# Kernel tuning notes

Hardware: AMD Instinct MI355X
Metric: run time of the kernel (lower is better)

The kernel has to match this reference:

```python
import jax, jax.numpy as jnp
import numpy as np

B, D, E, H, L = 32768, 512, 10, 128, 2  # batch, input_dim, max_charts, expert hidden, latent_dim
RH1, RH2 = 256, 128                      # router hidden sizes
TAU = 3.0


def setup_inputs() -> dict:
    key = jax.random.key(0)
    ks = jax.random.split(key, 16)
    rnd = lambda k, *s: (jax.random.normal(k, s, jnp.float32) * 0.05)
    return {
        "x": jax.random.normal(ks[0], (B, D), jnp.float32),
        "u": jax.random.uniform(ks[1], (B, E), jnp.float32),
        # router params (last layer init ~ N(0, 0.01), bias 0, as in _init_router)
        "rw1": rnd(ks[2], D, RH1), "rb1": jnp.zeros((RH1,), jnp.float32),
        "rw2": rnd(ks[3], RH1, RH2), "rb2": jnp.zeros((RH2,), jnp.float32),
        "rw3": jax.random.normal(ks[4], (RH2, E), jnp.float32) * 0.01,
        "rb3": jnp.zeros((E,), jnp.float32),
        # stacked expert params: all 10 experts batched along leading dim
        "ew1": rnd(ks[5], E, D, H), "eb1": rnd(ks[6], E, H),
        "ew2": rnd(ks[7], E, H, H), "eb2": rnd(ks[8], E, H),
        "ew3": rnd(ks[9], E, H, L), "eb3": rnd(ks[10], E, L),
    }


def reference(x, u, rw1, rb1, rw2, rb2, rw3, rb3, ew1, eb1, ew2, eb2, ew3, eb3):
    # router MLP: D -> 256 -> 128 -> E
    h = jax.nn.relu(x @ rw1 + rb1)
    h = jax.nn.relu(h @ rw2 + rb2)
    logits = h @ rw3 + rb3                                  # [B, E]
    # gumbel_softmax(tau=3.0, hard=False): softmax((logits + gumbel)/tau)
    g = -jnp.log(-jnp.log(jnp.clip(u, 1e-10, 1.0)) + 1e-10)
    weights = jax.nn.softmax((logits + g) / TAU, axis=1)    # [B, E]
    # all 10 experts as batched GEMMs (fuses the python loop over charts)
    h1 = jax.nn.relu(jnp.einsum('bi,eio->beo', x, ew1) + eb1[None])   # [B, E, H]
    h2 = jax.nn.relu(jnp.einsum('beh,eho->beo', h1, ew2) + eb2[None]) # [B, E, H]
    zc = jnp.einsum('beh,ehl->bel', h2, ew3) + eb3[None]              # [B, E, L]
    z = jnp.einsum('be,bel->bl', weights, zc)                         # [B, L]
    chart_outputs = jnp.transpose(zc, (1, 0, 2))                      # [E, B, L]
    return z, weights, chart_outputs
```

## Files before the change

kernel.cpp:

```cpp
#include <hip/hip_runtime.h>
#include <stdint.h>

typedef __bf16 bf16x8 __attribute__((ext_vector_type(8)));
typedef float floatx4 __attribute__((ext_vector_type(4)));
typedef unsigned short ushort_t;

__device__ __forceinline__ ushort_t bf16rne(float f) {
    union { float f; unsigned u; } v; v.f = f;
    return (ushort_t)((v.u + 0x7fffu + ((v.u >> 16) & 1u)) >> 16);
}

__device__ __forceinline__ void gl_lds16(const ushort_t* g, ushort_t* l) {
    __builtin_amdgcn_global_load_lds(
        (const __attribute__((address_space(1))) unsigned int*)g,
        (__attribute__((address_space(3))) unsigned int*)l, 16, 0, 0);
}


__global__ void prep(const float* __restrict__ x, ushort_t* __restrict__ x16,
                     const float* __restrict__ ew1, ushort_t* __restrict__ ew1t,
                     const float* __restrict__ ew2, ushort_t* __restrict__ ew2t,
                     const float* __restrict__ rw1, ushort_t* __restrict__ rw1t,
                     const float* __restrict__ rw2, ushort_t* __restrict__ rw2t) {
    __shared__ ushort_t sT[64 * 65];
    int b = blockIdx.x, tid = threadIdx.x;
    if (b < 16384) {
        int i = b * 256 + tid;
        float4 f = ((const float4*)x)[i];
        union { ushort_t s[4]; uint2 v; } pk;
        pk.s[0] = bf16rne(f.x); pk.s[1] = bf16rne(f.y);
        pk.s[2] = bf16rne(f.z); pk.s[3] = bf16rne(f.w);
        ((uint2*)x16)[i] = pk.v;
        return;
    }
    const float* in; ushort_t* outp; int K, N, k0, n0;
    int i = b - 16384;
    if (i < 160) {
        int e = i >> 4, t = i & 15;
        in = ew1 + e * 65536; outp = ew1t + e * 65536;
        K = 512; N = 128; k0 = (t >> 1) * 64; n0 = (t & 1) * 64;
    } else if (i < 200) {
        i -= 160; int e = i >> 2, t = i & 3;
        in = ew2 + e * 16384; outp = ew2t + e * 16384;
        K = 128; N = 128; k0 = (t >> 1) * 64; n0 = (t & 1) * 64;
    } else if (i < 232) {
        i -= 200; in = rw1; outp = rw1t;
        K = 512; N = 256; k0 = (i >> 2) * 64; n0 = (i & 3) * 64;
    } else {
        i -= 232; in = rw2; outp = rw2t;
        K = 256; N = 128; k0 = (i >> 1) * 64; n0 = (i & 1) * 64;
    }
    {
        int c = tid & 63, r0 = tid >> 6;
#pragma unroll
        for (int p = 0; p < 16; ++p) {
            int r = r0 * 16 + p;
            sT[c * 65 + r] = bf16rne(in[(size_t)(k0 + r) * N + n0 + c]);
        }
        __syncthreads();
        int rr = tid & 63, c0 = tid >> 6;
#pragma unroll
        for (int p = 0; p < 16; ++p) {
            int cc = c0 * 16 + p;
            outp[(size_t)(n0 + cc) * K + k0 + rr] = sT[cc * 65 + rr];
        }
    }
}

__global__ __launch_bounds__(256, 2)
void router_fused(const ushort_t* __restrict__ x16, const ushort_t* __restrict__ rw1t,
                  const float* __restrict__ rb1, const ushort_t* __restrict__ rw2t,
                  const float* __restrict__ rb2, const float* __restrict__ rw3,
                  const float* __restrict__ rb3, const float* __restrict__ u,
                  float* __restrict__ wts, float* __restrict__ z) {
    __shared__ alignas(16) ushort_t sStage[8192];
    __shared__ alignas(16) ushort_t sH1[16384];
    __shared__ float sw3[1280];
    __shared__ float sB1[128];
    __shared__ float sB2[128];
    __shared__ float lgbuf[128][10];

    const int tid = threadIdx.x;
    const int rb = blockIdx.x;
    const int wave = tid >> 6, lane = tid & 63;
    const int ln15 = lane & 15, q = lane >> 4;
    const int wm = (wave & 1) * 64, wn = (wave >> 1) * 64;
    const int mhalf = wm >> 6, nhalf = wn >> 6;

    for (int i = tid; i < 1280; i += 256) sw3[i] = rw3[i];
    if (tid < 128) sB2[tid] = rb2[tid];

    const ushort_t* xblk = x16 + (size_t)rb * 128 * 512;
    const int rl = lane >> 2, cl = lane & 3;
    const int sw = (cl ^ ((rl >> 1) & 3)) * 8;
    const int rg0 = wave * 2, rg1 = rg0 + 1;
    const int fslot = (4 * ln15 + (q ^ ((ln15 >> 1) & 3))) * 8;

    floatx4 acc2[4][4];
#pragma unroll
    for (int i = 0; i < 4; ++i)
#pragma unroll
        for (int j = 0; j < 4; ++j) acc2[i][j] = (floatx4){0.f, 0.f, 0.f, 0.f};

    for (int ph = 0; ph < 2; ++ph) {
        if (tid < 128) sB1[tid] = rb1[ph * 128 + tid];
        const ushort_t* w1base = rw1t + (size_t)ph * 128 * 512;

        floatx4 acc[4][4];
#pragma unroll
        for (int i = 0; i < 4; ++i)
#pragma unroll
            for (int j = 0; j < 4; ++j) acc[i][j] = (floatx4){0.f, 0.f, 0.f, 0.f};

        for (int k0 = 0; k0 < 512; k0 += 32) {
            __syncthreads();
            gl_lds16(xblk + (size_t)(rg0 * 16 + rl) * 512 + k0 + sw, &sStage[rg0 * 512]);
            gl_lds16(xblk + (size_t)(rg1 * 16 + rl) * 512 + k0 + sw, &sStage[rg1 * 512]);
            gl_lds16(w1base + (size_t)(rg0 * 16 + rl) * 512 + k0 + sw, &sStage[4096 + rg0 * 512]);
            gl_lds16(w1base + (size_t)(rg1 * 16 + rl) * 512 + k0 + sw, &sStage[4096 + rg1 * 512]);
            __syncthreads();
            bf16x8 a[4], b[4];
#pragma unroll
            for (int t = 0; t < 4; ++t) a[t] = *(const bf16x8*)(&sStage[4096 + (mhalf * 4 + t) * 512 + fslot]);
#pragma unroll
            for (int t = 0; t < 4; ++t) b[t] = *(const bf16x8*)(&sStage[(nhalf * 4 + t) * 512 + fslot]);
#pragma unroll
            for (int i = 0; i < 4; ++i)
#pragma unroll
                for (int j = 0; j < 4; ++j)
                    acc[i][j] = __builtin_amdgcn_mfma_f32_16x16x32_bf16(a[i], b[j], acc[i][j], 0, 0, 0);
        }

#pragma unroll
        for (int i = 0; i < 4; ++i) {
            int hbase = wm + 16 * i;
            int kh = hbase >> 5;
            int qhi = (hbase >> 4) & 1;
            int slotq = 2 * qhi + (q >> 1);
            int h0 = hbase + q * 4;
#pragma unroll
            for (int j = 0; j < 4; ++j) {
                union { ushort_t s[4]; uint2 v; } pk;
#pragma unroll
                for (int r = 0; r < 4; ++r)
                    pk.s[r] = bf16rne(fmaxf(acc[i][j][r] + sB1[h0 + r], 0.f));
                *(uint2*)(&sH1[kh * 4096 + (nhalf * 4 + j) * 512 + slotq * 128 + ln15 * 8 + (q & 1) * 4]) = pk.v;
            }
        }

        for (int p = 0; p < 2; ++p) {
            __syncthreads();
#pragma unroll
            for (int r = 0; r < 4; ++r) {
                int s = wave * 4 + r;
                int khl = s >> 3, rg = s & 7;
                int kh = p * 2 + khl;
                gl_lds16(rw2t + (size_t)(rg * 16 + rl) * 256 + ph * 128 + kh * 32 + sw, &sStage[s * 512]);
            }
            __syncthreads();
#pragma unroll
            for (int khl = 0; khl < 2; ++khl) {
                int kh = p * 2 + khl;
                bf16x8 a[4], b[4];
#pragma unroll
                for (int t = 0; t < 4; ++t) a[t] = *(const bf16x8*)(&sStage[(khl * 8 + mhalf * 4 + t) * 512 + fslot]);
#pragma unroll
                for (int t = 0; t < 4; ++t) b[t] = *(const bf16x8*)(&sH1[kh * 4096 + (nhalf * 4 + t) * 512 + lane * 8]);
#pragma unroll
                for (int i = 0; i < 4; ++i)
#pragma unroll
                    for (int j = 0; j < 4; ++j)
                        acc2[i][j] = __builtin_amdgcn_mfma_f32_16x16x32_bf16(a[i], b[j], acc2[i][j], 0, 0, 0);
            }
        }
    }

    float lg[4][10];
#pragma unroll
    for (int j = 0; j < 4; ++j)
#pragma unroll
        for (int ee = 0; ee < 10; ++ee) lg[j][ee] = 0.f;
#pragma unroll
    for (int i = 0; i < 4; ++i) {
#pragma unroll
        for (int r = 0; r < 4; ++r) {
            int n = wm + i * 16 + q * 4 + r;
            float bias = sB2[n];
            const float* w3r = &sw3[n * 10];
#pragma unroll
            for (int j = 0; j < 4; ++j) {
                float val = fmaxf(acc2[i][j][r] + bias, 0.f);
#pragma unroll
                for (int ee = 0; ee < 10; ++ee) lg[j][ee] += val * w3r[ee];
            }
        }
    }
#pragma unroll
    for (int j = 0; j < 4; ++j)
#pragma unroll
        for (int ee = 0; ee < 10; ++ee) {
            lg[j][ee] += __shfl_xor(lg[j][ee], 16, 64);
            lg[j][ee] += __shfl_xor(lg[j][ee], 32, 64);
        }
    if (wm == 0 && q == 0) {
#pragma unroll
        for (int j = 0; j < 4; ++j) {
            int row = wn + 16 * j + ln15;
#pragma unroll
            for (int ee = 0; ee < 10; ++ee) lgbuf[row][ee] = lg[j][ee];
        }
    }
    __syncthreads();
    if (wm == 64 && q == 0) {
#pragma unroll
        for (int j = 0; j < 4; ++j) {
            int row = wn + 16 * j + ln15;
#pragma unroll
            for (int ee = 0; ee < 10; ++ee) lgbuf[row][ee] += lg[j][ee];
        }
    }
    __syncthreads();
    if (tid < 128) {
        int grow = rb * 128 + tid;
        float v[10], mx = -1e30f;
#pragma unroll
        for (int ee = 0; ee < 10; ++ee) {
            float uu = u[(size_t)grow * 10 + ee];
            uu = fminf(fmaxf(uu, 1e-10f), 1.0f);
            float g = -logf(-logf(uu) + 1e-10f);
            v[ee] = (lgbuf[tid][ee] + rb3[ee] + g) * (1.0f / 3.0f);
            mx = fmaxf(mx, v[ee]);
        }
        float s = 0.f;
#pragma unroll
        for (int ee = 0; ee < 10; ++ee) { v[ee] = expf(v[ee] - mx); s += v[ee]; }
        float inv = 1.0f / s;
#pragma unroll
        for (int ee = 0; ee < 10; ++ee) wts[(size_t)grow * 10 + ee] = v[ee] * inv;
    }
    z[rb * 256 + tid] = 0.f;
}

__global__ __launch_bounds__(256, 3)
void expert_fused(const ushort_t* __restrict__ x16, const ushort_t* __restrict__ ew1t,
                  const ushort_t* __restrict__ ew2t, const float* __restrict__ eb1,
                  const float* __restrict__ eb2, const float* __restrict__ ew3,
                  const float* __restrict__ eb3, const float* __restrict__ wts,
                  float* __restrict__ chart, float* __restrict__ z) {
    __shared__ alignas(16) ushort_t sXW[8192];
    __shared__ alignas(16) ushort_t sH1[16384];
    __shared__ float sB1[128];
    __shared__ float sB2[128];
    __shared__ float sW3[256];
    __shared__ float zbuf[128][2];

    const int tid = threadIdx.x;
    const int id = blockIdx.x;
    const int xcd = id & 7, local = id >> 3;
    const int e = local % 10;
    const int rb = xcd * 32 + local / 10;

    const int wave = tid >> 6, lane = tid & 63;
    const int ln15 = lane & 15, q = lane >> 4;
    const int wm = (wave & 1) * 64, wn = (wave >> 1) * 64;
    const int mhalf = wm >> 6, nhalf = wn >> 6;

    if (tid < 128) sB1[tid] = eb1[e * 128 + tid];
    else sB2[tid - 128] = eb2[e * 128 + (tid - 128)];
    sW3[tid] = ew3[e * 256 + tid];

    const ushort_t* xblk = x16 + (size_t)rb * 128 * 512;
    const ushort_t* w1 = ew1t + (size_t)e * 128 * 512;
    const ushort_t* w2 = ew2t + (size_t)e * 128 * 128;

    const int rl = lane >> 2, cl = lane & 3;
    const int sw = (cl ^ ((rl >> 1) & 3)) * 8;
    const int rg0 = wave * 2, rg1 = rg0 + 1;
    const int fslot = (4 * ln15 + (q ^ ((ln15 >> 1) & 3))) * 8;

    {
        floatx4 acc[4][4];
#pragma unroll
        for (int i = 0; i < 4; ++i)
#pragma unroll
            for (int j = 0; j < 4; ++j) acc[i][j] = (floatx4){0.f, 0.f, 0.f, 0.f};

        for (int k0 = 0; k0 < 512; k0 += 32) {
            __syncthreads();
            gl_lds16(xblk + (size_t)(rg0 * 16 + rl) * 512 + k0 + sw, &sXW[rg0 * 512]);
            gl_lds16(xblk + (size_t)(rg1 * 16 + rl) * 512 + k0 + sw, &sXW[rg1 * 512]);
            gl_lds16(w1 + (size_t)(rg0 * 16 + rl) * 512 + k0 + sw, &sXW[4096 + rg0 * 512]);
            gl_lds16(w1 + (size_t)(rg1 * 16 + rl) * 512 + k0 + sw, &sXW[4096 + rg1 * 512]);
            __syncthreads();
            bf16x8 a[4], b[4];
#pragma unroll
            for (int t = 0; t < 4; ++t) a[t] = *(const bf16x8*)(&sXW[4096 + (mhalf * 4 + t) * 512 + fslot]);
#pragma unroll
            for (int t = 0; t < 4; ++t) b[t] = *(const bf16x8*)(&sXW[(nhalf * 4 + t) * 512 + fslot]);
#pragma unroll
            for (int i = 0; i < 4; ++i)
#pragma unroll
                for (int j = 0; j < 4; ++j)
                    acc[i][j] = __builtin_amdgcn_mfma_f32_16x16x32_bf16(a[i], b[j], acc[i][j], 0, 0, 0);
        }

#pragma unroll
        for (int i = 0; i < 4; ++i) {
            int hbase = wm + 16 * i;
            int kh = hbase >> 5;
            int qhi = (hbase >> 4) & 1;
            int slotq = 2 * qhi + (q >> 1);
            int h0 = hbase + q * 4;
#pragma unroll
            for (int j = 0; j < 4; ++j) {
                union { ushort_t s[4]; uint2 v; } pk;
#pragma unroll
                for (int r = 0; r < 4; ++r)
                    pk.s[r] = bf16rne(fmaxf(acc[i][j][r] + sB1[h0 + r], 0.f));
                *(uint2*)(&sH1[kh * 4096 + (nhalf * 4 + j) * 512 + slotq * 128 + ln15 * 8 + (q & 1) * 4]) = pk.v;
            }
        }
    }

    floatx4 acc2[4][4];
#pragma unroll
    for (int i = 0; i < 4; ++i)
#pragma unroll
        for (int j = 0; j < 4; ++j) acc2[i][j] = (floatx4){0.f, 0.f, 0.f, 0.f};

    for (int p = 0; p < 2; ++p) {
        __syncthreads();
#pragma unroll
        for (int r = 0; r < 4; ++r) {
            int s = wave * 4 + r;
            int khl = s >> 3, rg = s & 7;
            int kh = p * 2 + khl;
            gl_lds16(w2 + (size_t)(rg * 16 + rl) * 128 + kh * 32 + sw, &sXW[s * 512]);
        }
        __syncthreads();
#pragma unroll
        for (int khl = 0; khl < 2; ++khl) {
            int kh = p * 2 + khl;
            bf16x8 a[4], b[4];
#pragma unroll
            for (int t = 0; t < 4; ++t) a[t] = *(const bf16x8*)(&sXW[(khl * 8 + mhalf * 4 + t) * 512 + fslot]);
#pragma unroll
            for (int t = 0; t < 4; ++t) b[t] = *(const bf16x8*)(&sH1[kh * 4096 + (nhalf * 4 + t) * 512 + lane * 8]);
#pragma unroll
            for (int i = 0; i < 4; ++i)
#pragma unroll
                for (int j = 0; j < 4; ++j)
                    acc2[i][j] = __builtin_amdgcn_mfma_f32_16x16x32_bf16(a[i], b[j], acc2[i][j], 0, 0, 0);
        }
    }

    float zc0[4] = {0.f, 0.f, 0.f, 0.f}, zc1[4] = {0.f, 0.f, 0.f, 0.f};
#pragma unroll
    for (int i = 0; i < 4; ++i) {
        int o0 = wm + i * 16 + q * 4;
#pragma unroll
        for (int r = 0; r < 4; ++r) {
            int o = o0 + r;
            float w3a = sW3[2 * o], w3b = sW3[2 * o + 1];
            float bias = sB2[o];
#pragma unroll
            for (int j = 0; j < 4; ++j) {
                float val = fmaxf(acc2[i][j][r] + bias, 0.f);
                zc0[j] += val * w3a;
                zc1[j] += val * w3b;
            }
        }
    }
#pragma unroll
    for (int j = 0; j < 4; ++j) {
        zc0[j] += __shfl_xor(zc0[j], 16, 64);
        zc0[j] += __shfl_xor(zc0[j], 32, 64);
        zc1[j] += __shfl_xor(zc1[j], 16, 64);
        zc1[j] += __shfl_xor(zc1[j], 32, 64);
    }
    if (wm == 0 && q == 0) {
#pragma unroll
        for (int j = 0; j < 4; ++j) {
            int row = wn + j * 16 + ln15;
            zbuf[row][0] = zc0[j];
            zbuf[row][1] = zc1[j];
        }
    }
    __syncthreads();
    if (wm == 64 && q == 0) {
#pragma unroll
        for (int j = 0; j < 4; ++j) {
            int row = wn + j * 16 + ln15;
            zbuf[row][0] += zc0[j];
            zbuf[row][1] += zc1[j];
        }
    }
    __syncthreads();
    {
        int row = tid >> 1, l = tid & 1;
        int grow = rb * 128 + row;
        float vz = zbuf[row][l] + eb3[e * 2 + l];
        chart[(size_t)e * 65536 + (size_t)grow * 2 + l] = vz;
        atomicAdd(&z[(size_t)grow * 2 + l], wts[(size_t)grow * 10 + e] * vz);
    }
}

extern "C" void kernel_launch(void* const* d_in, const int* in_sizes, int n_in,
                              void* d_out, int out_size, void* d_ws, size_t ws_size,
                              hipStream_t stream) {
    const float* x = (const float*)d_in[0];
    const float* u = (const float*)d_in[1];
    const float* rw1 = (const float*)d_in[2];
    const float* rb1 = (const float*)d_in[3];
    const float* rw2 = (const float*)d_in[4];
    const float* rb2 = (const float*)d_in[5];
    const float* rw3 = (const float*)d_in[6];
    const float* rb3 = (const float*)d_in[7];
    const float* ew1 = (const float*)d_in[8];
    const float* eb1 = (const float*)d_in[9];
    const float* ew2 = (const float*)d_in[10];
    const float* eb2 = (const float*)d_in[11];
    const float* ew3 = (const float*)d_in[12];
    const float* eb3 = (const float*)d_in[13];
    float* out = (float*)d_out;
    float* z = out;
    float* wts = out + 65536;
    float* chart = out + 393216;

    ushort_t* x16  = (ushort_t*)d_ws;
    ushort_t* ew1t = x16 + 16777216;
    ushort_t* ew2t = ew1t + 655360;
    ushort_t* rw1t = ew2t + 163840;
    ushort_t* rw2t = rw1t + 131072;

    prep<<<16624, 256, 0, stream>>>(x, x16, ew1, ew1t, ew2, ew2t, rw1, rw1t, rw2, rw2t);

    router_fused<<<256, 256, 0, stream>>>(x16, rw1t, rb1, rw2t, rb2, rw3, rb3,
                                          u, wts, z);

    expert_fused<<<2560, 256, 0, stream>>>(x16, ew1t, ew2t, eb1, eb2, ew3, eb3,
                                           wts, chart, z);
}
```

Measured before the change: 220.5 us.

## Double-buffer x tiles in LDS and stream expert weights directly into registers

The expert kernel now double-buffers the x tile in LDS, so the next k-slice is fetched while MFMAs run on the current one. Expert weight fragments for both GEMMs are loaded straight from global memory into registers, ahead of use, instead of being staged through LDS. The W2 prefetch is issued during the last GEMM1 iteration, and the GEMM2 loop drops its per-step barriers. This aims to hide global latency and cut LDS traffic and barriers, at the cost of more registers (which may hurt occupancy under launch_bounds 3) and uncoalesced-ish per-lane weight reads that rely on the cache, since the same weights are reread across blocks.

```diff
diff --git a/kernel.cpp b/kernel.cpp
--- a/kernel.cpp
+++ b/kernel.cpp
@@ -247,7 +247,7 @@
                   const float* __restrict__ eb2, const float* __restrict__ ew3,
                   const float* __restrict__ eb3, const float* __restrict__ wts,
                   float* __restrict__ chart, float* __restrict__ z) {
-    __shared__ alignas(16) ushort_t sXW[8192];
+    __shared__ alignas(16) ushort_t sX[2][4096];
     __shared__ alignas(16) ushort_t sH1[16384];
     __shared__ float sB1[128];
     __shared__ float sB2[128];
@@ -263,21 +263,23 @@
     const int wave = tid >> 6, lane = tid & 63;
     const int ln15 = lane & 15, q = lane >> 4;
     const int wm = (wave & 1) * 64, wn = (wave >> 1) * 64;
-    const int mhalf = wm >> 6, nhalf = wn >> 6;
+    const int nhalf = wn >> 6;
 
     if (tid < 128) sB1[tid] = eb1[e * 128 + tid];
     else sB2[tid - 128] = eb2[e * 128 + (tid - 128)];
     sW3[tid] = ew3[e * 256 + tid];
 
     const ushort_t* xblk = x16 + (size_t)rb * 128 * 512;
-    const ushort_t* w1 = ew1t + (size_t)e * 128 * 512;
-    const ushort_t* w2 = ew2t + (size_t)e * 128 * 128;
+    const ushort_t* w1row = ew1t + (size_t)e * 65536 + (size_t)(wm + ln15) * 512 + q * 8;
+    const ushort_t* w2row = ew2t + (size_t)e * 16384 + (size_t)(wm + ln15) * 128 + q * 8;
 
     const int rl = lane >> 2, cl = lane & 3;
     const int sw = (cl ^ ((rl >> 1) & 3)) * 8;
     const int rg0 = wave * 2, rg1 = rg0 + 1;
     const int fslot = (4 * ln15 + (q ^ ((ln15 >> 1) & 3))) * 8;
 
+    bf16x8 a0[4], a1[4], wa0[4], wa1[4];
+
     {
         floatx4 acc[4][4];
 #pragma unroll
@@ -285,23 +287,49 @@
 #pragma unroll
             for (int j = 0; j < 4; ++j) acc[i][j] = (floatx4){0.f, 0.f, 0.f, 0.f};
 
-        for (int k0 = 0; k0 < 512; k0 += 32) {
-            __syncthreads();
-            gl_lds16(xblk + (size_t)(rg0 * 16 + rl) * 512 + k0 + sw, &sXW[rg0 * 512]);
-            gl_lds16(xblk + (size_t)(rg1 * 16 + rl) * 512 + k0 + sw, &sXW[rg1 * 512]);
-            gl_lds16(w1 + (size_t)(rg0 * 16 + rl) * 512 + k0 + sw, &sXW[4096 + rg0 * 512]);
-            gl_lds16(w1 + (size_t)(rg1 * 16 + rl) * 512 + k0 + sw, &sXW[4096 + rg1 * 512]);
-            __syncthreads();
-            bf16x8 a[4], b[4];
-#pragma unroll
-            for (int t = 0; t < 4; ++t) a[t] = *(const bf16x8*)(&sXW[4096 + (mhalf * 4 + t) * 512 + fslot]);
-#pragma unroll
-            for (int t = 0; t < 4; ++t) b[t] = *(const bf16x8*)(&sXW[(nhalf * 4 + t) * 512 + fslot]);
-#pragma unroll
-            for (int i = 0; i < 4; ++i)
-#pragma unroll
-                for (int j = 0; j < 4; ++j)
-                    acc[i][j] = __builtin_amdgcn_mfma_f32_16x16x32_bf16(a[i], b[j], acc[i][j], 0, 0, 0);
+        gl_lds16(xblk + (size_t)(rg0 * 16 + rl) * 512 + sw, &sX[0][rg0 * 512]);
+        gl_lds16(xblk + (size_t)(rg1 * 16 + rl) * 512 + sw, &sX[0][rg1 * 512]);
+#pragma unroll
+        for (int t = 0; t < 4; ++t) a0[t] = *(const bf16x8*)(w1row + t * 8192);
+
+#pragma unroll
+        for (int kk = 0; kk < 8; ++kk) {
+            const int k0 = kk * 64;
+            __syncthreads();
+            gl_lds16(xblk + (size_t)(rg0 * 16 + rl) * 512 + (k0 + 32) + sw, &sX[1][rg0 * 512]);
+            gl_lds16(xblk + (size_t)(rg1 * 16 + rl) * 512 + (k0 + 32) + sw, &sX[1][rg1 * 512]);
+#pragma unroll
+            for (int t = 0; t < 4; ++t) a1[t] = *(const bf16x8*)(w1row + t * 8192 + k0 + 32);
+            {
+                bf16x8 b[4];
+#pragma unroll
+                for (int t = 0; t < 4; ++t) b[t] = *(const bf16x8*)(&sX[0][(nhalf * 4 + t) * 512 + fslot]);
+#pragma unroll
+                for (int i = 0; i < 4; ++i)
+#pragma unroll
+                    for (int j = 0; j < 4; ++j)
+                        acc[i][j] = __builtin_amdgcn_mfma_f32_16x16x32_bf16(a0[i], b[j], acc[i][j], 0, 0, 0);
+            }
+            __syncthreads();
+            if (kk < 7) {
+                gl_lds16(xblk + (size_t)(rg0 * 16 + rl) * 512 + (k0 + 64) + sw, &sX[0][rg0 * 512]);
+                gl_lds16(xblk + (size_t)(rg1 * 16 + rl) * 512 + (k0 + 64) + sw, &sX[0][rg1 * 512]);
+#pragma unroll
+                for (int t = 0; t < 4; ++t) a0[t] = *(const bf16x8*)(w1row + t * 8192 + k0 + 64);
+            } else {
+#pragma unroll
+                for (int t = 0; t < 4; ++t) wa0[t] = *(const bf16x8*)(w2row + t * 2048);
+            }
+            {
+                bf16x8 b[4];
+#pragma unroll
+                for (int t = 0; t < 4; ++t) b[t] = *(const bf16x8*)(&sX[1][(nhalf * 4 + t) * 512 + fslot]);
+#pragma unroll
+                for (int i = 0; i < 4; ++i)
+#pragma unroll
+                    for (int j = 0; j < 4; ++j)
+                        acc[i][j] = __builtin_amdgcn_mfma_f32_16x16x32_bf16(a1[i], b[j], acc[i][j], 0, 0, 0);
+            }
         }
 
 #pragma unroll
@@ -328,29 +356,35 @@
 #pragma unroll
         for (int j = 0; j < 4; ++j) acc2[i][j] = (floatx4){0.f, 0.f, 0.f, 0.f};
 
-    for (int p = 0; p < 2; ++p) {
-        __syncthreads();
-#pragma unroll
-        for (int r = 0; r < 4; ++r) {
-            int s = wave * 4 + r;
-            int khl = s >> 3, rg = s & 7;
-            int kh = p * 2 + khl;
-            gl_lds16(w2 + (size_t)(rg * 16 + rl) * 128 + kh * 32 + sw, &sXW[s * 512]);
-        }
-        __syncthreads();
-#pragma unroll
-        for (int khl = 0; khl < 2; ++khl) {
-            int kh = p * 2 + khl;
-            bf16x8 a[4], b[4];
-#pragma unroll
-            for (int t = 0; t < 4; ++t) a[t] = *(const bf16x8*)(&sXW[(khl * 8 + mhalf * 4 + t) * 512 + fslot]);
+    __syncthreads();
+#pragma unroll
+    for (int kp = 0; kp < 2; ++kp) {
+        const int kh = kp * 2;
+#pragma unroll
+        for (int t = 0; t < 4; ++t) wa1[t] = *(const bf16x8*)(w2row + t * 2048 + (kh + 1) * 32);
+        {
+            bf16x8 b[4];
 #pragma unroll
             for (int t = 0; t < 4; ++t) b[t] = *(const bf16x8*)(&sH1[kh * 4096 + (nhalf * 4 + t) * 512 + lane * 8]);
 #pragma unroll
             for (int i = 0; i < 4; ++i)
 #pragma unroll
                 for (int j = 0; j < 4; ++j)
-                    acc2[i][j] = __builtin_amdgcn_mfma_f32_16x16x32_bf16(a[i], b[j], acc2[i][j], 0, 0, 0);
+                    acc2[i][j] = __builtin_amdgcn_mfma_f32_16x16x32_bf16(wa0[i], b[j], acc2[i][j], 0, 0, 0);
+        }
+        if (kp < 1) {
+#pragma unroll
+            for (int t = 0; t < 4; ++t) wa0[t] = *(const bf16x8*)(w2row + t * 2048 + (kh + 2) * 32);
+        }
+        {
+            bf16x8 b[4];
+#pragma unroll
+            for (int t = 0; t < 4; ++t) b[t] = *(const bf16x8*)(&sH1[(kh + 1) * 4096 + (nhalf * 4 + t) * 512 + lane * 8]);
+#pragma unroll
+            for (int i = 0; i < 4; ++i)
+#pragma unroll
+                for (int j = 0; j < 4; ++j)
+                    acc2[i][j] = __builtin_amdgcn_mfma_f32_16x16x32_bf16(wa1[i], b[j], acc2[i][j], 0, 0, 0);
         }
     }
 
```

Result: slower. 263.8 us (+19.6%).

## Merge router and expert kernels into one grid, compute z in separate pass

Applied to the files above, without the earlier changes.

Router and expert work now run in a single launch: the first 256 blocks compute the router MLP and softmax weights, the remaining 2560 blocks compute the per-expert MLPs. This removes the dependency that forced the expert kernel to wait for the router, so router blocks can overlap with expert blocks. The atomicAdd into z is replaced by a small z_final kernel that reads the weights and chart outputs and writes z directly. The router branch now runs at higher occupancy bounds and reuses the staging buffer for rw3 and logits, which may raise register pressure in that path.

```diff
diff --git a/kernel.cpp b/kernel.cpp
--- a/kernel.cpp
+++ b/kernel.cpp
@@ -67,86 +67,250 @@
     }
 }
 
-__global__ __launch_bounds__(256, 2)
-void router_fused(const ushort_t* __restrict__ x16, const ushort_t* __restrict__ rw1t,
-                  const float* __restrict__ rb1, const ushort_t* __restrict__ rw2t,
-                  const float* __restrict__ rb2, const float* __restrict__ rw3,
-                  const float* __restrict__ rb3, const float* __restrict__ u,
-                  float* __restrict__ wts, float* __restrict__ z) {
-    __shared__ alignas(16) ushort_t sStage[8192];
+__global__ __launch_bounds__(256, 3)
+void fused_main(const ushort_t* __restrict__ x16,
+                const ushort_t* __restrict__ rw1t, const float* __restrict__ rb1,
+                const ushort_t* __restrict__ rw2t, const float* __restrict__ rb2,
+                const float* __restrict__ rw3, const float* __restrict__ rb3,
+                const float* __restrict__ u,
+                const ushort_t* __restrict__ ew1t, const ushort_t* __restrict__ ew2t,
+                const float* __restrict__ eb1, const float* __restrict__ eb2,
+                const float* __restrict__ ew3, const float* __restrict__ eb3,
+                float* __restrict__ wts, float* __restrict__ chart) {
+    __shared__ alignas(16) ushort_t sXW[8192];
     __shared__ alignas(16) ushort_t sH1[16384];
-    __shared__ float sw3[1280];
     __shared__ float sB1[128];
     __shared__ float sB2[128];
-    __shared__ float lgbuf[128][10];
+    __shared__ float sW3e[256];
+    __shared__ float zbuf[128][2];
 
     const int tid = threadIdx.x;
-    const int rb = blockIdx.x;
+    const int id = blockIdx.x;
     const int wave = tid >> 6, lane = tid & 63;
     const int ln15 = lane & 15, q = lane >> 4;
     const int wm = (wave & 1) * 64, wn = (wave >> 1) * 64;
     const int mhalf = wm >> 6, nhalf = wn >> 6;
-
-    for (int i = tid; i < 1280; i += 256) sw3[i] = rw3[i];
-    if (tid < 128) sB2[tid] = rb2[tid];
-
-    const ushort_t* xblk = x16 + (size_t)rb * 128 * 512;
     const int rl = lane >> 2, cl = lane & 3;
     const int sw = (cl ^ ((rl >> 1) & 3)) * 8;
     const int rg0 = wave * 2, rg1 = rg0 + 1;
     const int fslot = (4 * ln15 + (q ^ ((ln15 >> 1) & 3))) * 8;
 
-    floatx4 acc2[4][4];
-#pragma unroll
-    for (int i = 0; i < 4; ++i)
-#pragma unroll
-        for (int j = 0; j < 4; ++j) acc2[i][j] = (floatx4){0.f, 0.f, 0.f, 0.f};
-
-    for (int ph = 0; ph < 2; ++ph) {
-        if (tid < 128) sB1[tid] = rb1[ph * 128 + tid];
-        const ushort_t* w1base = rw1t + (size_t)ph * 128 * 512;
-
-        floatx4 acc[4][4];
+    if (id < 256) {
+        const int rb = id;
+        if (tid < 128) sB2[tid] = rb2[tid];
+        const ushort_t* xblk = x16 + (size_t)rb * 128 * 512;
+
+        floatx4 acc2[4][4];
 #pragma unroll
         for (int i = 0; i < 4; ++i)
 #pragma unroll
-            for (int j = 0; j < 4; ++j) acc[i][j] = (floatx4){0.f, 0.f, 0.f, 0.f};
-
-        for (int k0 = 0; k0 < 512; k0 += 32) {
-            __syncthreads();
-            gl_lds16(xblk + (size_t)(rg0 * 16 + rl) * 512 + k0 + sw, &sStage[rg0 * 512]);
-            gl_lds16(xblk + (size_t)(rg1 * 16 + rl) * 512 + k0 + sw, &sStage[rg1 * 512]);
-            gl_lds16(w1base + (size_t)(rg0 * 16 + rl) * 512 + k0 + sw, &sStage[4096 + rg0 * 512]);
-            gl_lds16(w1base + (size_t)(rg1 * 16 + rl) * 512 + k0 + sw, &sStage[4096 + rg1 * 512]);
-            __syncthreads();
-            bf16x8 a[4], b[4];
-#pragma unroll
-            for (int t = 0; t < 4; ++t) a[t] = *(const bf16x8*)(&sStage[4096 + (mhalf * 4 + t) * 512 + fslot]);
-#pragma unroll
-            for (int t = 0; t < 4; ++t) b[t] = *(const bf16x8*)(&sStage[(nhalf * 4 + t) * 512 + fslot]);
+            for (int j = 0; j < 4; ++j) acc2[i][j] = (floatx4){0.f, 0.f, 0.f, 0.f};
+
+        for (int ph = 0; ph < 2; ++ph) {
+            if (tid < 128) sB1[tid] = rb1[ph * 128 + tid];
+            const ushort_t* w1base = rw1t + (size_t)ph * 128 * 512;
+
+            floatx4 acc[4][4];
 #pragma unroll
             for (int i = 0; i < 4; ++i)
 #pragma unroll
-                for (int j = 0; j < 4; ++j)
-                    acc[i][j] = __builtin_amdgcn_mfma_f32_16x16x32_bf16(a[i], b[j], acc[i][j], 0, 0, 0);
-        }
-
+                for (int j = 0; j < 4; ++j) acc[i][j] = (floatx4){0.f, 0.f, 0.f, 0.f};
+
+            for (int k0 = 0; k0 < 512; k0 += 32) {
+                __syncthreads();
+                gl_lds16(xblk + (size_t)(rg0 * 16 + rl) * 512 + k0 + sw, &sXW[rg0 * 512]);
+                gl_lds16(xblk + (size_t)(rg1 * 16 + rl) * 512 + k0 + sw, &sXW[rg1 * 512]);
+                gl_lds16(w1base + (size_t)(rg0 * 16 + rl) * 512 + k0 + sw, &sXW[4096 + rg0 * 512]);
+                gl_lds16(w1base + (size_t)(rg1 * 16 + rl) * 512 + k0 + sw, &sXW[4096 + rg1 * 512]);
+                __syncthreads();
+                bf16x8 a[4], b[4];
+#pragma unroll
+                for (int t = 0; t < 4; ++t) a[t] = *(const bf16x8*)(&sXW[4096 + (mhalf * 4 + t) * 512 + fslot]);
+#pragma unroll
+                for (int t = 0; t < 4; ++t) b[t] = *(const bf16x8*)(&sXW[(nhalf * 4 + t) * 512 + fslot]);
+#pragma unroll
+                for (int i = 0; i < 4; ++i)
+#pragma unroll
+                    for (int j = 0; j < 4; ++j)
+                        acc[i][j] = __builtin_amdgcn_mfma_f32_16x16x32_bf16(a[i], b[j], acc[i][j], 0, 0, 0);
+            }
+
+#pragma unroll
+            for (int i = 0; i < 4; ++i) {
+                int hbase = wm + 16 * i;
+                int kh = hbase >> 5;
+                int qhi = (hbase >> 4) & 1;
+                int slotq = 2 * qhi + (q >> 1);
+                int h0 = hbase + q * 4;
+#pragma unroll
+                for (int j = 0; j < 4; ++j) {
+                    union { ushort_t s[4]; uint2 v; } pk;
+#pragma unroll
+                    for (int r = 0; r < 4; ++r)
+                        pk.s[r] = bf16rne(fmaxf(acc[i][j][r] + sB1[h0 + r], 0.f));
+                    *(uint2*)(&sH1[kh * 4096 + (nhalf * 4 + j) * 512 + slotq * 128 + ln15 * 8 + (q & 1) * 4]) = pk.v;
+                }
+            }
+
+            for (int p = 0; p < 2; ++p) {
+                __syncthreads();
+#pragma unroll
+                for (int r = 0; r < 4; ++r) {
+                    int s = wave * 4 + r;
+                    int khl = s >> 3, rg = s & 7;
+                    int kh = p * 2 + khl;
+                    gl_lds16(rw2t + (size_t)(rg * 16 + rl) * 256 + ph * 128 + kh * 32 + sw, &sXW[s * 512]);
+                }
+                __syncthreads();
+#pragma unroll
+                for (int khl = 0; khl < 2; ++khl) {
+                    int kh = p * 2 + khl;
+                    bf16x8 a[4], b[4];
+#pragma unroll
+                    for (int t = 0; t < 4; ++t) a[t] = *(const bf16x8*)(&sXW[(khl * 8 + mhalf * 4 + t) * 512 + fslot]);
+#pragma unroll
+                    for (int t = 0; t < 4; ++t) b[t] = *(const bf16x8*)(&sH1[kh * 4096 + (nhalf * 4 + t) * 512 + lane * 8]);
+#pragma unroll
+                    for (int i = 0; i < 4; ++i)
+#pragma unroll
+                        for (int j = 0; j < 4; ++j)
+                            acc2[i][j] = __builtin_amdgcn_mfma_f32_16x16x32_bf16(a[i], b[j], acc2[i][j], 0, 0, 0);
+                }
+            }
+        }
+
+        __syncthreads();
+        float* sw3r = (float*)sXW;
+        float* lgbuf = (float*)(&sXW[2560]);
+        for (int i = tid; i < 1280; i += 256) sw3r[i] = rw3[i];
+        __syncthreads();
+
+        float lg[4][10];
+#pragma unroll
+        for (int j = 0; j < 4; ++j)
+#pragma unroll
+            for (int ee = 0; ee < 10; ++ee) lg[j][ee] = 0.f;
 #pragma unroll
         for (int i = 0; i < 4; ++i) {
-            int hbase = wm + 16 * i;
-            int kh = hbase >> 5;
-            int qhi = (hbase >> 4) & 1;
-            int slotq = 2 * qhi + (q >> 1);
-            int h0 = hbase + q * 4;
+#pragma unroll
+            for (int r = 0; r < 4; ++r) {
+                int n = wm + i * 16 + q * 4 + r;
+                float bias = sB2[n];
+                const float* w3r = &sw3r[n * 10];
+#pragma unroll
+                for (int j = 0; j < 4; ++j) {
+                    float val = fmaxf(acc2[i][j][r] + bias, 0.f);
+#pragma unroll
+                    for (int ee = 0; ee < 10; ++ee) lg[j][ee] += val * w3r[ee];
+                }
+            }
+        }
+#pragma unroll
+        for (int j = 0; j < 4; ++j)
+#pragma unroll
+            for (int ee = 0; ee < 10; ++ee) {
+                lg[j][ee] += __shfl_xor(lg[j][ee], 16, 64);
+                lg[j][ee] += __shfl_xor(lg[j][ee], 32, 64);
+            }
+        if (wm == 0 && q == 0) {
 #pragma unroll
             for (int j = 0; j < 4; ++j) {
-                union { ushort_t s[4]; uint2 v; } pk;
-#pragma unroll
-                for (int r = 0; r < 4; ++r)
-                    pk.s[r] = bf16rne(fmaxf(acc[i][j][r] + sB1[h0 + r], 0.f));
-                *(uint2*)(&sH1[kh * 4096 + (nhalf * 4 + j) * 512 + slotq * 128 + ln15 * 8 + (q & 1) * 4]) = pk.v;
-            }
-        }
+                int row = wn + 16 * j + ln15;
+#pragma unroll
+                for (int ee = 0; ee < 10; ++ee) lgbuf[row * 10 + ee] = lg[j][ee];
+            }
+        }
+        __syncthreads();
+        if (wm == 64 && q == 0) {
+#pragma unroll
+            for (int j = 0; j < 4; ++j) {
+                int row = wn + 16 * j + ln15;
+#pragma unroll
+                for (int ee = 0; ee < 10; ++ee) lgbuf[row * 10 + ee] += lg[j][ee];
+            }
+        }
+        __syncthreads();
+        if (tid < 128) {
+            int grow = rb * 128 + tid;
+            float v[10], mx = -1e30f;
+#pragma unroll
+            for (int ee = 0; ee < 10; ++ee) {
+                float uu = u[(size_t)grow * 10 + ee];
+                uu = fminf(fmaxf(uu, 1e-10f), 1.0f);
+                float g = -logf(-logf(uu) + 1e-10f);
+                v[ee] = (lgbuf[tid * 10 + ee] + rb3[ee] + g) * (1.0f / 3.0f);
+                mx = fmaxf(mx, v[ee]);
+            }
+            float s = 0.f;
+#pragma unroll
+            for (int ee = 0; ee < 10; ++ee) { v[ee] = expf(v[ee] - mx); s += v[ee]; }
+            float inv = 1.0f / s;
+#pragma unroll
+            for (int ee = 0; ee < 10; ++ee) wts[(size_t)grow * 10 + ee] = v[ee] * inv;
+        }
+    } else {
+        const int eid = id - 256;
+        const int xcd = eid & 7, local = eid >> 3;
+        const int e = local % 10;
+        const int rb = xcd * 32 + local / 10;
+
+        if (tid < 128) sB1[tid] = eb1[e * 128 + tid];
+        else sB2[tid - 128] = eb2[e * 128 + (tid - 128)];
+        sW3e[tid] = ew3[e * 256 + tid];
+
+        const ushort_t* xblk = x16 + (size_t)rb * 128 * 512;
+        const ushort_t* w1 = ew1t + (size_t)e * 128 * 512;
+        const ushort_t* w2 = ew2t + (size_t)e * 128 * 128;
+
+        {
+            floatx4 acc[4][4];
+#pragma unroll
+            for (int i = 0; i < 4; ++i)
+#pragma unroll
+                for (int j = 0; j < 4; ++j) acc[i][j] = (floatx4){0.f, 0.f, 0.f, 0.f};
+
+            for (int k0 = 0; k0 < 512; k0 += 32) {
+                __syncthreads();
+                gl_lds16(xblk + (size_t)(rg0 * 16 + rl) * 512 + k0 + sw, &sXW[rg0 * 512]);
+                gl_lds16(xblk + (size_t)(rg1 * 16 + rl) * 512 + k0 + sw, &sXW[rg1 * 512]);
+                gl_lds16(w1 + (size_t)(rg0 * 16 + rl) * 512 + k0 + sw, &sXW[4096 + rg0 * 512]);
+                gl_lds16(w1 + (size_t)(rg1 * 16 + rl) * 512 + k0 + sw, &sXW[4096 + rg1 * 512]);
+                __syncthreads();
+                bf16x8 a[4], b[4];
+#pragma unroll
+                for (int t = 0; t < 4; ++t) a[t] = *(const bf16x8*)(&sXW[4096 + (mhalf * 4 + t) * 512 + fslot]);
+#pragma unroll
+                for (int t = 0; t < 4; ++t) b[t] = *(const bf16x8*)(&sXW[(nhalf * 4 + t) * 512 + fslot]);
+#pragma unroll
+                for (int i = 0; i < 4; ++i)
+#pragma unroll
+                    for (int j = 0; j < 4; ++j)
+                        acc[i][j] = __builtin_amdgcn_mfma_f32_16x16x32_bf16(a[i], b[j], acc[i][j], 0, 0, 0);
+            }
+
+#pragma unroll
+            for (int i = 0; i < 4; ++i) {
+                int hbase = wm + 16 * i;
+                int kh = hbase >> 5;
+                int qhi = (hbase >> 4) & 1;
+                int slotq = 2 * qhi + (q >> 1);
+                int h0 = hbase + q * 4;
+#pragma unroll
+                for (int j = 0; j < 4; ++j) {
+                    union { ushort_t s[4]; uint2 v; } pk;
+#pragma unroll
+                    for (int r = 0; r < 4; ++r)
+                        pk.s[r] = bf16rne(fmaxf(acc[i][j][r] + sB1[h0 + r], 0.f));
+                    *(uint2*)(&sH1[kh * 4096 + (nhalf * 4 + j) * 512 + slotq * 128 + ln15 * 8 + (q & 1) * 4]) = pk.v;
+                }
+            }
+        }
+
+        floatx4 acc2[4][4];
+#pragma unroll
+        for (int i = 0; i < 4; ++i)
+#pragma unroll
+            for (int j = 0; j < 4; ++j) acc2[i][j] = (floatx4){0.f, 0.f, 0.f, 0.f};
 
         for (int p = 0; p < 2; ++p) {
             __syncthreads();
@@ -155,7 +319,7 @@
                 int s = wave * 4 + r;
                 int khl = s >> 3, rg = s & 7;
                 int kh = p * 2 + khl;
-                gl_lds16(rw2t + (size_t)(rg * 16 + rl) * 256 + ph * 128 + kh * 32 + sw, &sStage[s * 512]);
+                gl_lds16(w2 + (size_t)(rg * 16 + rl) * 128 + kh * 32 + sw, &sXW[s * 512]);
             }
             __syncthreads();
 #pragma unroll
@@ -163,7 +327,7 @@
                 int kh = p * 2 + khl;
                 bf16x8 a[4], b[4];
 #pragma unroll
-                for (int t = 0; t < 4; ++t) a[t] = *(const bf16x8*)(&sStage[(khl * 8 + mhalf * 4 + t) * 512 + fslot]);
+                for (int t = 0; t < 4; ++t) a[t] = *(const bf16x8*)(&sXW[(khl * 8 + mhalf * 4 + t) * 512 + fslot]);
 #pragma unroll
                 for (int t = 0; t < 4; ++t) b[t] = *(const bf16x8*)(&sH1[kh * 4096 + (nhalf * 4 + t) * 512 + lane * 8]);
 #pragma unroll
@@ -173,236 +337,70 @@
                         acc2[i][j] = __builtin_amdgcn_mfma_f32_16x16x32_bf16(a[i], b[j], acc2[i][j], 0, 0, 0);
             }
         }
+
+        float zc0[4] = {0.f, 0.f, 0.f, 0.f}, zc1[4] = {0.f, 0.f, 0.f, 0.f};
+#pragma unroll
+        for (int i = 0; i < 4; ++i) {
+            int o0 = wm + i * 16 + q * 4;
+#pragma unroll
+            for (int r = 0; r < 4; ++r) {
+                int o = o0 + r;
+                float w3a = sW3e[2 * o], w3b = sW3e[2 * o + 1];
+                float bias = sB2[o];
+#pragma unroll
+                for (int j = 0; j < 4; ++j) {
+                    float val = fmaxf(acc2[i][j][r] + bias, 0.f);
+                    zc0[j] += val * w3a;
+                    zc1[j] += val * w3b;
+                }
+            }
+        }
+#pragma unroll
+        for (int j = 0; j < 4; ++j) {
+            zc0[j] += __shfl_xor(zc0[j], 16, 64);
+            zc0[j] += __shfl_xor(zc0[j], 32, 64);
+            zc1[j] += __shfl_xor(zc1[j], 16, 64);
+            zc1[j] += __shfl_xor(zc1[j], 32, 64);
+        }
+        if (wm == 0 && q == 0) {
+#pragma unroll
+            for (int j = 0; j < 4; ++j) {
+                int row = wn + j * 16 + ln15;
+                zbuf[row][0] = zc0[j];
+                zbuf[row][1] = zc1[j];
+            }
+        }
+        __syncthreads();
+        if (wm == 64 && q == 0) {
+#pragma unroll
+            for (int j = 0; j < 4; ++j) {
+                int row = wn + j * 16 + ln15;
+                zbuf[row][0] += zc0[j];
+                zbuf[row][1] += zc1[j];
+            }
+        }
+        __syncthreads();
+        {
+            int row = tid >> 1, l = tid & 1;
+            int grow = rb * 128 + row;
+            chart[(size_t)e * 65536 + (size_t)grow * 2 + l] = zbuf[row][l] + eb3[e * 2 + l];
+        }
     }
-
-    float lg[4][10];
-#pragma unroll
-    for (int j = 0; j < 4; ++j)
-#pragma unroll
-        for (int ee = 0; ee < 10; ++ee) lg[j][ee] = 0.f;
-#pragma unroll
-    for (int i = 0; i < 4; ++i) {
-#pragma unroll
-        for (int r = 0; r < 4; ++r) {
-            int n = wm + i * 16 + q * 4 + r;
-            float bias = sB2[n];
-            const float* w3r = &sw3[n * 10];
-#pragma unroll
-            for (int j = 0; j < 4; ++j) {
-                float val = fmaxf(acc2[i][j][r] + bias, 0.f);
-#pragma unroll
-                for (int ee = 0; ee < 10; ++ee) lg[j][ee] += val * w3r[ee];
-            }
-        }
+}
+
+__global__ void z_final(const float* __restrict__ w, const float* __restrict__ chart,
+                        float* __restrict__ z) {
+    int row = blockIdx.x * 256 + threadIdx.x;
+    float z0 = 0.f, z1 = 0.f;
+#pragma unroll
+    for (int e = 0; e < 10; ++e) {
+        float we = w[(size_t)row * 10 + e];
+        float2 c = *(const float2*)(&chart[(size_t)e * 65536 + (size_t)row * 2]);
+        z0 += we * c.x;
+        z1 += we * c.y;
     }
-#pragma unroll
-    for (int j = 0; j < 4; ++j)
-#pragma unroll
-        for (int ee = 0; ee < 10; ++ee) {
-            lg[j][ee] += __shfl_xor(lg[j][ee], 16, 64);
-            lg[j][ee] += __shfl_xor(lg[j][ee], 32, 64);
-        }
-    if (wm == 0 && q == 0) {
-#pragma unroll
-        for (int j = 0; j < 4; ++j) {
-            int row = wn + 16 * j + ln15;
-#pragma unroll
-            for (int ee = 0; ee < 10; ++ee) lgbuf[row][ee] = lg[j][ee];
-        }
-    }
-    __syncthreads();
-    if (wm == 64 && q == 0) {
-#pragma unroll
-        for (int j = 0; j < 4; ++j) {
-            int row = wn + 16 * j + ln15;
-#pragma unroll
-            for (int ee = 0; ee < 10; ++ee) lgbuf[row][ee] += lg[j][ee];
-        }
-    }
-    __syncthreads();
-    if (tid < 128) {
-        int grow = rb * 128 + tid;
-        float v[10], mx = -1e30f;
-#pragma unroll
-        for (int ee = 0; ee < 10; ++ee) {
-            float uu = u[(size_t)grow * 10 + ee];
-            uu = fminf(fmaxf(uu, 1e-10f), 1.0f);
-            float g = -logf(-logf(uu) + 1e-10f);
-            v[ee] = (lgbuf[tid][ee] + rb3[ee] + g) * (1.0f / 3.0f);
-            mx = fmaxf(mx, v[ee]);
-        }
-        float s = 0.f;
-#pragma unroll
-        for (int ee = 0; ee < 10; ++ee) { v[ee] = expf(v[ee] - mx); s += v[ee]; }
-        float inv = 1.0f / s;
-#pragma unroll
-        for (int ee = 0; ee < 10; ++ee) wts[(size_t)grow * 10 + ee] = v[ee] * inv;
-    }
-    z[rb * 256 + tid] = 0.f;
-}
-
-__global__ __launch_bounds__(256, 3)
-void expert_fused(const ushort_t* __restrict__ x16, const ushort_t* __restrict__ ew1t,
-                  const ushort_t* __restrict__ ew2t, const float* __restrict__ eb1,
-                  const float* __restrict__ eb2, const float* __restrict__ ew3,
-                  const float* __restrict__ eb3, const float* __restrict__ wts,
-                  float* __restrict__ chart, float* __restrict__ z) {
-    __shared__ alignas(16) ushort_t sXW[8192];
-    __shared__ alignas(16) ushort_t sH1[16384];
-    __shared__ float sB1[128];
-    __shared__ float sB2[128];
-    __shared__ float sW3[256];
-    __shared__ float zbuf[128][2];
-
-    const int tid = threadIdx.x;
-    const int id = blockIdx.x;
-    const int xcd = id & 7, local = id >> 3;
-    const int e = local % 10;
-    const int rb = xcd * 32 + local / 10;
-
-    const int wave = tid >> 6, lane = tid & 63;
-    const int ln15 = lane & 15, q = lane >> 4;
-    const int wm = (wave & 1) * 64, wn = (wave >> 1) * 64;
-    const int mhalf = wm >> 6, nhalf = wn >> 6;
-
-    if (tid < 128) sB1[tid] = eb1[e * 128 + tid];
-    else sB2[tid - 128] = eb2[e * 128 + (tid - 128)];
-    sW3[tid] = ew3[e * 256 + tid];
-
-    const ushort_t* xblk = x16 + (size_t)rb * 128 * 512;
-    const ushort_t* w1 = ew1t + (size_t)e * 128 * 512;
-    const ushort_t* w2 = ew2t + (size_t)e * 128 * 128;
-
-    const int rl = lane >> 2, cl = lane & 3;
-    const int sw = (cl ^ ((rl >> 1) & 3)) * 8;
-    const int rg0 = wave * 2, rg1 = rg0 + 1;
-    const int fslot = (4 * ln15 + (q ^ ((ln15 >> 1) & 3))) * 8;
-
-    {
-        floatx4 acc[4][4];
-#pragma unroll
-        for (int i = 0; i < 4; ++i)
-#pragma unroll
-            for (int j = 0; j < 4; ++j) acc[i][j] = (floatx4){0.f, 0.f, 0.f, 0.f};
-
-        for (int k0 = 0; k0 < 512; k0 += 32) {
-            __syncthreads();
-            gl_lds16(xblk + (size_t)(rg0 * 16 + rl) * 512 + k0 + sw, &sXW[rg0 * 512]);
-            gl_lds16(xblk + (size_t)(rg1 * 16 + rl) * 512 + k0 + sw, &sXW[rg1 * 512]);
-            gl_lds16(w1 + (size_t)(rg0 * 16 + rl) * 512 + k0 + sw, &sXW[4096 + rg0 * 512]);
-            gl_lds16(w1 + (size_t)(rg1 * 16 + rl) * 512 + k0 + sw, &sXW[4096 + rg1 * 512]);
-            __syncthreads();
-            bf16x8 a[4], b[4];
-#pragma unroll
-            for (int t = 0; t < 4; ++t) a[t] = *(const bf16x8*)(&sXW[4096 + (mhalf * 4 + t) * 512 + fslot]);
-#pragma unroll
-            for (int t = 0; t < 4; ++t) b[t] = *(const bf16x8*)(&sXW[(nhalf * 4 + t) * 512 + fslot]);
-#pragma unroll
-            for (int i = 0; i < 4; ++i)
-#pragma unroll
-                for (int j = 0; j < 4; ++j)
-                    acc[i][j] = __builtin_amdgcn_mfma_f32_16x16x32_bf16(a[i], b[j], acc[i][j], 0, 0, 0);
-        }
-
-#pragma unroll
-        for (int i = 0; i < 4; ++i) {
-            int hbase = wm + 16 * i;
-            int kh = hbase >> 5;
-            int qhi = (hbase >> 4) & 1;
-            int slotq = 2 * qhi + (q >> 1);
-            int h0 = hbase + q * 4;
-#pragma unroll
-            for (int j = 0; j < 4; ++j) {
-                union { ushort_t s[4]; uint2 v; } pk;
-#pragma unroll
-                for (int r = 0; r < 4; ++r)
-                    pk.s[r] = bf16rne(fmaxf(acc[i][j][r] + sB1[h0 + r], 0.f));
-                *(uint2*)(&sH1[kh * 4096 + (nhalf * 4 + j) * 512 + slotq * 128 + ln15 * 8 + (q & 1) * 4]) = pk.v;
-            }
-        }
-    }
-
-    floatx4 acc2[4][4];
-#pragma unroll
-    for (int i = 0; i < 4; ++i)
-#pragma unroll
-        for (int j = 0; j < 4; ++j) acc2[i][j] = (floatx4){0.f, 0.f, 0.f, 0.f};
-
-    for (int p = 0; p < 2; ++p) {
-        __syncthreads();
-#pragma unroll
-        for (int r = 0; r < 4; ++r) {
-            int s = wave * 4 + r;
-            int khl = s >> 3, rg = s & 7;
-            int kh = p * 2 + khl;
-            gl_lds16(w2 + (size_t)(rg * 16 + rl) * 128 + kh * 32 + sw, &sXW[s * 512]);
-        }
-        __syncthreads();
-#pragma unroll
-        for (int khl = 0; khl < 2; ++khl) {
-            int kh = p * 2 + khl;
-            bf16x8 a[4], b[4];
-#pragma unroll
-            for (int t = 0; t < 4; ++t) a[t] = *(const bf16x8*)(&sXW[(khl * 8 + mhalf * 4 + t) * 512 + fslot]);
-#pragma unroll
-            for (int t = 0; t < 4; ++t) b[t] = *(const bf16x8*)(&sH1[kh * 4096 + (nhalf * 4 + t) * 512 + lane * 8]);
-#pragma unroll
-            for (int i = 0; i < 4; ++i)
-#pragma unroll
-                for (int j = 0; j < 4; ++j)
-                    acc2[i][j] = __builtin_amdgcn_mfma_f32_16x16x32_bf16(a[i], b[j], acc2[i][j], 0, 0, 0);
-        }
-    }
-
-    float zc0[4] = {0.f, 0.f, 0.f, 0.f}, zc1[4] = {0.f, 0.f, 0.f, 0.f};
-#pragma unroll
-    for (int i = 0; i < 4; ++i) {
-        int o0 = wm + i * 16 + q * 4;
-#pragma unroll
-        for (int r = 0; r < 4; ++r) {
-            int o = o0 + r;
-            float w3a = sW3[2 * o], w3b = sW3[2 * o + 1];
-            float bias = sB2[o];
-#pragma unroll
-            for (int j = 0; j < 4; ++j) {
-                float val = fmaxf(acc2[i][j][r] + bias, 0.f);
-                zc0[j] += val * w3a;
-                zc1[j] += val * w3b;
-            }
-        }
-    }
-#pragma unroll
-    for (int j = 0; j < 4; ++j) {
-        zc0[j] += __shfl_xor(zc0[j], 16, 64);
-        zc0[j] += __shfl_xor(zc0[j], 32, 64);
-        zc1[j] += __shfl_xor(zc1[j], 16, 64);
-        zc1[j] += __shfl_xor(zc1[j], 32, 64);
-    }
-    if (wm == 0 && q == 0) {
-#pragma unroll
-        for (int j = 0; j < 4; ++j) {
-            int row = wn + j * 16 + ln15;
-            zbuf[row][0] = zc0[j];
-            zbuf[row][1] = zc1[j];
-        }
-    }
-    __syncthreads();
-    if (wm == 64 && q == 0) {
-#pragma unroll
-        for (int j = 0; j < 4; ++j) {
-            int row = wn + j * 16 + ln15;
-            zbuf[row][0] += zc0[j];
-            zbuf[row][1] += zc1[j];
-        }
-    }
-    __syncthreads();
-    {
-        int row = tid >> 1, l = tid & 1;
-        int grow = rb * 128 + row;
-        float vz = zbuf[row][l] + eb3[e * 2 + l];
-        chart[(size_t)e * 65536 + (size_t)grow * 2 + l] = vz;
-        atomicAdd(&z[(size_t)grow * 2 + l], wts[(size_t)grow * 10 + e] * vz);
-    }
+    float2 o; o.x = z0; o.y = z1;
+    *(float2*)(&z[(size_t)row * 2]) = o;
 }
 
 extern "C" void kernel_launch(void* const* d_in, const int* in_sizes, int n_in,
@@ -435,9 +433,9 @@
 
     prep<<<16624, 256, 0, stream>>>(x, x16, ew1, ew1t, ew2, ew2t, rw1, rw1t, rw2, rw2t);
 
-    router_fused<<<256, 256, 0, stream>>>(x16, rw1t, rb1, rw2t, rb2, rw3, rb3,
-                                          u, wts, z);
-
-    expert_fused<<<2560, 256, 0, stream>>>(x16, ew1t, ew2t, eb1, eb2, ew3, eb3,
-                                           wts, chart, z);
-}
+    fused_main<<<2816, 256, 0, stream>>>(x16, rw1t, rb1, rw2t, rb2, rw3, rb3, u,
+                                         ew1t, ew2t, eb1, eb2, ew3, eb3,
+                                         wts, chart);
+
+    z_final<<<128, 256, 0, stream>>>(wts, chart, z);
+}
```

After: 222.0 us. No clear change (+0.7%).
